# Performance work log

Hardware: AMD Instinct MI355X
Metric: run time of the kernel (lower is better)

The kernel has to match this reference:

```python
import jax, jax.numpy as jnp
import numpy as np


def _segment_mean(x, idx, num_segments):
    # mean-aggregate rows of x into num_segments buckets (PyG SAGEConv default aggr)
    s = jax.ops.segment_sum(x, idx, num_segments=num_segments)
    c = jax.ops.segment_sum(jnp.ones((idx.shape[0],), x.dtype), idx, num_segments=num_segments)
    return s / jnp.maximum(c, 1.0)[:, None]


def setup_inputs() -> dict:
    key = jax.random.key(0)
    ks = jax.random.split(key, 12)
    N_LIG, N_PROT, D, H, E = 100000, 50000, 64, 128, 2000000
    sc = 0.05
    return {
        "x_lig": jax.random.normal(ks[0], (N_LIG, D), jnp.float32),
        "x_prot": jax.random.normal(ks[1], (N_PROT, D), jnp.float32),
        "W_l_lp": jax.random.normal(ks[2], (D, H), jnp.float32) * sc,
        "b_lp": jnp.zeros((H,), jnp.float32),
        "W_r_lp": jax.random.normal(ks[3], (D, H), jnp.float32) * sc,
        "W_l_pl": jax.random.normal(ks[4], (D, H), jnp.float32) * sc,
        "b_pl": jnp.zeros((H,), jnp.float32),
        "W_r_pl": jax.random.normal(ks[5], (D, H), jnp.float32) * sc,
        "W_lin": jax.random.normal(ks[6], (H, 1), jnp.float32) * sc,
        "b_lin": jnp.zeros((1,), jnp.float32),
        "src_lp": jax.random.randint(ks[7], (E,), 0, N_LIG, jnp.int32),
        "dst_lp": jax.random.randint(ks[8], (E,), 0, N_PROT, jnp.int32),
        "src_pl": jax.random.randint(ks[9], (E,), 0, N_PROT, jnp.int32),
        "dst_pl": jax.random.randint(ks[10], (E,), 0, N_LIG, jnp.int32),
    }


def reference(x_lig, x_prot, W_l_lp, b_lp, W_r_lp, W_l_pl, b_pl, W_r_pl,
              W_lin, b_lin, src_lp, dst_lp, src_pl, dst_pl):
    n_lig = x_lig.shape[0]
    n_prot = x_prot.shape[0]
    # SAGEConv ('ligand','interacts','protein'): gather ligand feats along edges, mean into proteins
    agg_prot = _segment_mean(x_lig[src_lp], dst_lp, n_prot)          # [N_prot, D]
    h_prot = jax.nn.relu(agg_prot @ W_l_lp + b_lp + x_prot @ W_r_lp)  # [N_prot, H] (dead downstream, as in original)
    # SAGEConv ('protein','interacts','ligand')
    agg_lig = _segment_mean(x_prot[src_pl], dst_pl, n_lig)           # [N_lig, D]
    h_lig = jax.nn.relu(agg_lig @ W_l_pl + b_pl + x_lig @ W_r_pl)    # [N_lig, H]
    ligand_out = h_lig.mean(axis=0)                                  # [H]
    del h_prot  # original computes it but never uses it (only 'ligand' feeds the head)
    return ligand_out @ W_lin + b_lin                                # [1]
```

## Files before the change

kernel.cpp:

```cpp
#include <hip/hip_runtime.h>

#define D 64
#define H 128
#define BN 128
#define CAP 3456
#define NBB 256
#define CE 7816

typedef short bf16x8 __attribute__((ext_vector_type(8)));
typedef float f32x4  __attribute__((ext_vector_type(4)));

__device__ __forceinline__ ushort f2bf(float f) {
    unsigned u = __float_as_uint(f);
    unsigned r = (u + 0x7FFFu + ((u >> 16) & 1u)) >> 16;
    return (ushort)r;
}

__device__ __forceinline__ bf16x8 pack8(float4 a, float4 b) {
    ushort o[8];
    o[0]=f2bf(a.x); o[1]=f2bf(a.y); o[2]=f2bf(a.z); o[3]=f2bf(a.w);
    o[4]=f2bf(b.x); o[5]=f2bf(b.y); o[6]=f2bf(b.z); o[7]=f2bf(b.w);
    bf16x8 r;
    __builtin_memcpy(&r, o, 16);
    return r;
}

__device__ __forceinline__ void accu(float* a, uint4 v) {
    a[0] += __uint_as_float(v.x << 16); a[1] += __uint_as_float(v.x & 0xFFFF0000u);
    a[2] += __uint_as_float(v.y << 16); a[3] += __uint_as_float(v.y & 0xFFFF0000u);
    a[4] += __uint_as_float(v.z << 16); a[5] += __uint_as_float(v.z & 0xFFFF0000u);
    a[6] += __uint_as_float(v.w << 16); a[7] += __uint_as_float(v.w & 0xFFFF0000u);
}

__global__ __launch_bounds__(256)
void stage1_kernel(const float* __restrict__ xp, ushort* __restrict__ xpb, int totalp,
                   const float* __restrict__ Wl, const float* __restrict__ Wr,
                   ushort* __restrict__ wprep,
                   const int* __restrict__ dst, int* __restrict__ cnt,
                   int E, int K, int ce, int PB) {
    __shared__ int scnt[800];
    int bid = blockIdx.x;
    int t = threadIdx.x;
    if (bid < PB) {
        int i = (bid * 256 + t) * 8;
        if (i < totalp) {
            float4 a = *(const float4*)(xp + i);
            float4 b = *(const float4*)(xp + i + 4);
            bf16x8 v = pack8(a, b);
            *(bf16x8*)(xpb + i) = v;
        }
    } else if (bid < PB + 8) {
        int e = (bid - PB) * 256 + t;
        if (e < 2048) {
            int lane = e & 63;
            int ks = (e >> 6) & 3;
            int ht = e >> 8;
            int h = ht * 16 + (lane & 15);
            int k0 = ks * 32 + (lane >> 4) * 8;
            ushort o[8];
            #pragma unroll
            for (int j = 0; j < 8; ++j) {
                int k = k0 + j;
                float v = (k < D) ? Wl[k * H + h] : Wr[(k - D) * H + h];
                o[j] = f2bf(v);
            }
            *(bf16x8*)(wprep + (size_t)e * 8) = *(bf16x8*)o;
        }
    } else {
        int blk = bid - PB - 8;
        for (int b = t; b < 800; b += 256) scnt[b] = 0;
        __syncthreads();
        int e0 = blk * ce;
        int e1 = min(E, e0 + ce);
        for (int i = e0 + t * 4; i < e1; i += 1024) {
            int4 d4 = *(const int4*)(dst + i);
            atomicAdd(&scnt[d4.x >> 7], 1);
            atomicAdd(&scnt[d4.y >> 7], 1);
            atomicAdd(&scnt[d4.z >> 7], 1);
            atomicAdd(&scnt[d4.w >> 7], 1);
        }
        __syncthreads();
        int* row = cnt + (size_t)blk * K;
        for (int b = t; b < K; b += 256) row[b] = scnt[b];
    }
}

__global__ __launch_bounds__(NBB)
void part_scan_kernel(const int* __restrict__ cnt, int* __restrict__ off,
                      int* __restrict__ tot, int K) {
    __shared__ int s[NBB];
    int b = blockIdx.x;
    int t = threadIdx.x;
    int v = cnt[(size_t)t * K + b];
    s[t] = v;
    __syncthreads();
    for (int o = 1; o < NBB; o <<= 1) {
        int x = (t >= o) ? s[t - o] : 0;
        __syncthreads();
        s[t] += x;
        __syncthreads();
    }
    off[(size_t)t * K + b] = s[t] - v;
    if (t == NBB - 1) tot[b] = s[t];
}

__global__ __launch_bounds__(512)
void part_scatter_kernel(const int* __restrict__ src, const int* __restrict__ dst,
                         const int* __restrict__ off, int* __restrict__ gb,
                         int E, int K, int ce) {
    __shared__ int shist[800];
    __shared__ int sbase[800];
    __shared__ int gdelta[800];
    __shared__ int lcur[800];
    __shared__ int sscan[512];
    __shared__ int ebuf[CE];
    __shared__ unsigned short bkt[CE];

    int blk = blockIdx.x, t = threadIdx.x;
    int e0 = blk * ce;
    int e1 = min(E, e0 + ce);
    int myn = e1 - e0;

    for (int b = t; b < 800; b += 512) shist[b] = 0;
    __syncthreads();
    for (int i = e0 + t * 4; i < e1; i += 2048) {
        int4 d4 = *(const int4*)(dst + i);
        atomicAdd(&shist[d4.x >> 7], 1);
        atomicAdd(&shist[d4.y >> 7], 1);
        atomicAdd(&shist[d4.z >> 7], 1);
        atomicAdd(&shist[d4.w >> 7], 1);
    }
    __syncthreads();
    int c0 = 0, c1 = 0;
    if (t < 400) { c0 = shist[2 * t]; c1 = shist[2 * t + 1]; }
    int cs = c0 + c1;
    sscan[t] = (t < 400) ? cs : 0;
    __syncthreads();
    for (int o = 1; o < 512; o <<= 1) {
        int x = (t >= o) ? sscan[t - o] : 0;
        __syncthreads();
        sscan[t] += x;
        __syncthreads();
    }
    if (t < 400) {
        int ex = sscan[t] - cs;
        sbase[2 * t] = ex;
        sbase[2 * t + 1] = ex + c0;
    }
    __syncthreads();
    const int* orow = off + (size_t)blk * K;
    for (int b = t; b < K; b += 512) {
        int sb = sbase[b];
        gdelta[b] = orow[b] - sb;
        lcur[b] = sb;
    }
    __syncthreads();
    for (int i = e0 + t * 4; i < e1; i += 2048) {
        int4 d4 = *(const int4*)(dst + i);
        int4 s4 = *(const int4*)(src + i);
        int b, p;
        b = d4.x >> 7; p = atomicAdd(&lcur[b], 1);
        ebuf[p] = (s4.x & 0xFFFF) | ((d4.x & 127) << 16); bkt[p] = (unsigned short)b;
        b = d4.y >> 7; p = atomicAdd(&lcur[b], 1);
        ebuf[p] = (s4.y & 0xFFFF) | ((d4.y & 127) << 16); bkt[p] = (unsigned short)b;
        b = d4.z >> 7; p = atomicAdd(&lcur[b], 1);
        ebuf[p] = (s4.z & 0xFFFF) | ((d4.z & 127) << 16); bkt[p] = (unsigned short)b;
        b = d4.w >> 7; p = atomicAdd(&lcur[b], 1);
        ebuf[p] = (s4.w & 0xFFFF) | ((d4.w & 127) << 16); bkt[p] = (unsigned short)b;
    }
    __syncthreads();
    for (int p = t; p < myn; p += 512) {
        int b = bkt[p];
        int loc = gdelta[b] + p;
        if (loc < CAP) gb[(size_t)b * CAP + loc] = ebuf[p];
    }
}

__global__ __launch_bounds__(512, 4)
void fused_kernel(const ushort* __restrict__ xpb, const float* __restrict__ x_lig,
                  const int* __restrict__ gtot, const int* __restrict__ gb,
                  const ushort* __restrict__ wprep, const float* __restrict__ bvec,
                  float* __restrict__ pgrid, int N) {
    __shared__ int sdeg[BN];
    __shared__ int sstart[BN];
    __shared__ int scur[BN];
    __shared__ int ssc[BN];
    __shared__ int scsr[CAP];
    __shared__ float sred[8][H];

    int b = blockIdx.x, t = threadIdx.x;
    int cnt = min(gtot[b], CAP);
    const int* mygb = gb + (size_t)b * CAP;

    if (t < BN) sdeg[t] = 0;
    __syncthreads();
    for (int i = t; i < cnt; i += 512)
        atomicAdd(&sdeg[mygb[i] >> 16], 1);
    __syncthreads();
    if (t < BN) ssc[t] = sdeg[t];
    __syncthreads();
    for (int off = 1; off < BN; off <<= 1) {
        int v = 0;
        if (t < BN && t >= off) v = ssc[t - off];
        __syncthreads();
        if (t < BN) ssc[t] += v;
        __syncthreads();
    }
    if (t < BN) {
        int ex = ssc[t] - sdeg[t];
        sstart[t] = ex;
        scur[t] = ex;
    }
    __syncthreads();
    for (int i = t; i < cnt; i += 512) {
        int e = mygb[i];
        int p = atomicAdd(&scur[e >> 16], 1);
        scsr[p] = e & 0xFFFF;
    }
    __syncthreads();

    int wv = t >> 6, lane = t & 63;
    int r = lane & 15, kg = lane >> 4;

    int ln = wv * 16 + r;
    int s0 = sstart[ln], dg = sdeg[ln];
    float a0[8] = {0.f,0.f,0.f,0.f,0.f,0.f,0.f,0.f};
    float a1[8] = {0.f,0.f,0.f,0.f,0.f,0.f,0.f,0.f};
    int j = 0;
    for (; j + 1 < dg; j += 2) {
        int i0 = scsr[s0 + j];
        int i1 = scsr[s0 + j + 1];
        const ushort* r0 = xpb + (size_t)i0 * D + kg * 8;
        const ushort* r1 = xpb + (size_t)i1 * D + kg * 8;
        uint4 u0 = *(const uint4*)(r0);
        uint4 u1 = *(const uint4*)(r0 + 32);
        uint4 w0 = *(const uint4*)(r1);
        uint4 w1 = *(const uint4*)(r1 + 32);
        accu(a0, u0); accu(a1, u1);
        accu(a0, w0); accu(a1, w1);
    }
    if (j < dg) {
        int i0 = scsr[s0 + j];
        const ushort* r0 = xpb + (size_t)i0 * D + kg * 8;
        uint4 u0 = *(const uint4*)(r0);
        uint4 u1 = *(const uint4*)(r0 + 32);
        accu(a0, u0); accu(a1, u1);
    }

    float inv = 1.0f / fmaxf((float)dg, 1.0f);
    ushort o0[8], o1[8];
    #pragma unroll
    for (int k = 0; k < 8; ++k) {
        o0[k] = f2bf(a0[k] * inv);
        o1[k] = f2bf(a1[k] * inv);
    }
    bf16x8 A0, A1;
    __builtin_memcpy(&A0, o0, 16);
    __builtin_memcpy(&A1, o1, 16);

    int grow = b * BN + wv * 16 + r;
    bf16x8 A2, A3;
    if (grow < N) {
        const float* xr = x_lig + (size_t)grow * D;
        float4 va = *(const float4*)(xr + kg * 8);
        float4 vb = *(const float4*)(xr + kg * 8 + 4);
        A2 = pack8(va, vb);
        float4 vc = *(const float4*)(xr + 32 + kg * 8);
        float4 vd = *(const float4*)(xr + 32 + kg * 8 + 4);
        A3 = pack8(vc, vd);
    } else {
        A2 = bf16x8{0,0,0,0,0,0,0,0};
        A3 = A2;
    }

    float hsum[8];
    bool full = (b * BN + wv * 16 + 16 <= N);
    const bf16x8* wp = (const bf16x8*)wprep;
    #pragma unroll 2
    for (int ht = 0; ht < 8; ++ht) {
        f32x4 acc = {0.f, 0.f, 0.f, 0.f};
        acc = __builtin_amdgcn_mfma_f32_16x16x32_bf16(A0, wp[(ht*4+0)*64 + lane], acc, 0, 0, 0);
        acc = __builtin_amdgcn_mfma_f32_16x16x32_bf16(A1, wp[(ht*4+1)*64 + lane], acc, 0, 0, 0);
        acc = __builtin_amdgcn_mfma_f32_16x16x32_bf16(A2, wp[(ht*4+2)*64 + lane], acc, 0, 0, 0);
        acc = __builtin_amdgcn_mfma_f32_16x16x32_bf16(A3, wp[(ht*4+3)*64 + lane], acc, 0, 0, 0);
        float bb = bvec[ht * 16 + r];
        float s = 0.f;
        if (full) {
            #pragma unroll
            for (int i = 0; i < 4; ++i) s += fmaxf(acc[i] + bb, 0.f);
        } else {
            #pragma unroll
            for (int i = 0; i < 4; ++i) {
                int row = b * BN + wv * 16 + kg * 4 + i;
                if (row < N) s += fmaxf(acc[i] + bb, 0.f);
            }
        }
        hsum[ht] = s;
    }

    #pragma unroll
    for (int ht = 0; ht < 8; ++ht) {
        float v = hsum[ht];
        v += __shfl_xor(v, 16);
        v += __shfl_xor(v, 32);
        if (lane < 16) sred[wv][ht * 16 + lane] = v;
    }
    __syncthreads();
    if (t < H) {
        float s = 0.f;
        #pragma unroll
        for (int w = 0; w < 8; ++w) s += sred[w][t];
        pgrid[(size_t)b * H + t] = s;
    }
}

__global__ __launch_bounds__(128)
void reduce1_kernel(const float* __restrict__ pgrid, int nb, float* __restrict__ pgrid2) {
    int t = threadIdx.x;
    float s = 0.f;
    for (int r = blockIdx.x; r < nb; r += 64) s += pgrid[(size_t)r * H + t];
    pgrid2[(size_t)blockIdx.x * H + t] = s;
}

__global__ __launch_bounds__(128)
void head_kernel(const float* __restrict__ pgrid2,
                 const float* __restrict__ W_lin, const float* __restrict__ b_lin,
                 float* __restrict__ out, float invN) {
    __shared__ float sh[H];
    int t = threadIdx.x;
    float s = 0.f;
    #pragma unroll 8
    for (int r = 0; r < 64; ++r) s += pgrid2[(size_t)r * H + t];
    sh[t] = s * invN * W_lin[t];
    __syncthreads();
    if (t == 0) {
        float tot = b_lin[0];
        for (int i = 0; i < H; ++i) tot += sh[i];
        out[0] = tot;
    }
}

extern "C" void kernel_launch(void* const* d_in, const int* in_sizes, int n_in,
                              void* d_out, int out_size, void* d_ws, size_t ws_size,
                              hipStream_t stream) {
    const float* x_lig  = (const float*)d_in[0];
    const float* x_prot = (const float*)d_in[1];
    const float* W_l_pl = (const float*)d_in[5];
    const float* b_pl   = (const float*)d_in[6];
    const float* W_r_pl = (const float*)d_in[7];
    const float* W_lin  = (const float*)d_in[8];
    const float* b_lin  = (const float*)d_in[9];
    const int*   src_pl = (const int*)d_in[12];
    const int*   dst_pl = (const int*)d_in[13];

    int N  = in_sizes[0] / D;
    int NP = in_sizes[1] / D;
    int E  = in_sizes[12];
    int K  = (N + BN - 1) / BN;

    char* base = (char*)d_ws;
    ushort* xpb   = (ushort*)base;  base += (size_t)NP * D * sizeof(ushort);
    float* pgrid  = (float*)base;   base += (size_t)K * H * sizeof(float);
    float* pgrid2 = (float*)base;   base += (size_t)64 * H * sizeof(float);
    ushort* wprep = (ushort*)base;  base += (size_t)2048 * 8 * sizeof(ushort);
    int* cnt      = (int*)base;     base += (size_t)NBB * K * sizeof(int);
    int* off      = (int*)base;     base += (size_t)NBB * K * sizeof(int);
    int* tot      = (int*)base;     base += (size_t)K * sizeof(int);
    base = (char*)(((size_t)base + 255) & ~(size_t)255);
    int* gb       = (int*)base;     base += (size_t)K * CAP * sizeof(int);

    int ce = ((E + NBB - 1) / NBB + 3) & ~3;
    int PB = (NP * D / 8 + 255) / 256;

    stage1_kernel<<<PB + 8 + NBB, 256, 0, stream>>>(x_prot, xpb, NP * D,
                                                    W_l_pl, W_r_pl, wprep,
                                                    dst_pl, cnt, E, K, ce, PB);
    part_scan_kernel<<<K, NBB, 0, stream>>>(cnt, off, tot, K);
    part_scatter_kernel<<<NBB, 512, 0, stream>>>(src_pl, dst_pl, off, gb, E, K, ce);
    fused_kernel<<<K, 512, 0, stream>>>(xpb, x_lig, tot, gb, wprep, b_pl, pgrid, N);
    reduce1_kernel<<<64, 128, 0, stream>>>(pgrid, K, pgrid2);
    head_kernel<<<1, 128, 0, stream>>>(pgrid2, W_lin, b_lin, (float*)d_out,
                                       1.0f / (float)N);
}
```

Measured before the change: 95.94 us.

## Store protein features as FP8 for gather, unroll gather by four, raise occupancy

The protein feature table is now converted to FP8 (e4m3) instead of bf16, which halves the bytes fetched per gathered neighbor row. The gather loop is unrolled to four edges and accumulates with packed FP8-to-f32 conversions. The weight prep is permuted so its K ordering matches the new interleaved layout of the aggregated features. Nontemporal loads are added for streamed data, and the launch bound is raised to 8 blocks per CU. FP8 quantization of the inputs loses a lot of precision, which may push the result outside the tolerance.

```diff
diff --git a/kernel.cpp b/kernel.cpp
--- a/kernel.cpp
+++ b/kernel.cpp
@@ -9,6 +9,7 @@
 
 typedef short bf16x8 __attribute__((ext_vector_type(8)));
 typedef float f32x4  __attribute__((ext_vector_type(4)));
+typedef float f32x2  __attribute__((ext_vector_type(2)));
 
 __device__ __forceinline__ ushort f2bf(float f) {
     unsigned u = __float_as_uint(f);
@@ -16,24 +17,34 @@
     return (ushort)r;
 }
 
-__device__ __forceinline__ bf16x8 pack8(float4 a, float4 b) {
+__device__ __forceinline__ bf16x8 pack8v(f32x4 a, f32x4 b) {
     ushort o[8];
-    o[0]=f2bf(a.x); o[1]=f2bf(a.y); o[2]=f2bf(a.z); o[3]=f2bf(a.w);
-    o[4]=f2bf(b.x); o[5]=f2bf(b.y); o[6]=f2bf(b.z); o[7]=f2bf(b.w);
+    o[0]=f2bf(a[0]); o[1]=f2bf(a[1]); o[2]=f2bf(a[2]); o[3]=f2bf(a[3]);
+    o[4]=f2bf(b[0]); o[5]=f2bf(b[1]); o[6]=f2bf(b[2]); o[7]=f2bf(b[3]);
     bf16x8 r;
     __builtin_memcpy(&r, o, 16);
     return r;
 }
 
-__device__ __forceinline__ void accu(float* a, uint4 v) {
-    a[0] += __uint_as_float(v.x << 16); a[1] += __uint_as_float(v.x & 0xFFFF0000u);
-    a[2] += __uint_as_float(v.y << 16); a[3] += __uint_as_float(v.y & 0xFFFF0000u);
-    a[4] += __uint_as_float(v.z << 16); a[5] += __uint_as_float(v.z & 0xFFFF0000u);
-    a[6] += __uint_as_float(v.w << 16); a[7] += __uint_as_float(v.w & 0xFFFF0000u);
+__device__ __forceinline__ void acc16(f32x2* a, uint4 v) {
+    a[0] += __builtin_amdgcn_cvt_pk_f32_fp8((int)v.x, false);
+    a[1] += __builtin_amdgcn_cvt_pk_f32_fp8((int)v.x, true);
+    a[2] += __builtin_amdgcn_cvt_pk_f32_fp8((int)v.y, false);
+    a[3] += __builtin_amdgcn_cvt_pk_f32_fp8((int)v.y, true);
+    a[4] += __builtin_amdgcn_cvt_pk_f32_fp8((int)v.z, false);
+    a[5] += __builtin_amdgcn_cvt_pk_f32_fp8((int)v.z, true);
+    a[6] += __builtin_amdgcn_cvt_pk_f32_fp8((int)v.w, false);
+    a[7] += __builtin_amdgcn_cvt_pk_f32_fp8((int)v.w, true);
+}
+
+__device__ __forceinline__ unsigned pk4_fp8(float x0, float x1, float x2, float x3) {
+    int w = __builtin_amdgcn_cvt_pk_fp8_f32(x0, x1, 0, false);
+    w = __builtin_amdgcn_cvt_pk_fp8_f32(x2, x3, w, true);
+    return (unsigned)w;
 }
 
 __global__ __launch_bounds__(256)
-void stage1_kernel(const float* __restrict__ xp, ushort* __restrict__ xpb, int totalp,
+void stage1_kernel(const float* __restrict__ xp, unsigned char* __restrict__ xp8, int totalp,
                    const float* __restrict__ Wl, const float* __restrict__ Wr,
                    ushort* __restrict__ wprep,
                    const int* __restrict__ dst, int* __restrict__ cnt,
@@ -42,12 +53,19 @@
     int bid = blockIdx.x;
     int t = threadIdx.x;
     if (bid < PB) {
-        int i = (bid * 256 + t) * 8;
+        int i = (bid * 256 + t) * 16;
         if (i < totalp) {
-            float4 a = *(const float4*)(xp + i);
-            float4 b = *(const float4*)(xp + i + 4);
-            bf16x8 v = pack8(a, b);
-            *(bf16x8*)(xpb + i) = v;
+            const f32x4* p = (const f32x4*)(xp + i);
+            f32x4 a = __builtin_nontemporal_load(p);
+            f32x4 b = __builtin_nontemporal_load(p + 1);
+            f32x4 c = __builtin_nontemporal_load(p + 2);
+            f32x4 d = __builtin_nontemporal_load(p + 3);
+            uint4 o;
+            o.x = pk4_fp8(a[0], a[1], a[2], a[3]);
+            o.y = pk4_fp8(b[0], b[1], b[2], b[3]);
+            o.z = pk4_fp8(c[0], c[1], c[2], c[3]);
+            o.w = pk4_fp8(d[0], d[1], d[2], d[3]);
+            *(uint4*)(xp8 + i) = o;
         }
     } else if (bid < PB + 8) {
         int e = (bid - PB) * 256 + t;
@@ -56,11 +74,12 @@
             int ks = (e >> 6) & 3;
             int ht = e >> 8;
             int h = ht * 16 + (lane & 15);
-            int k0 = ks * 32 + (lane >> 4) * 8;
+            int kgp = lane >> 4;
             ushort o[8];
             #pragma unroll
             for (int j = 0; j < 8; ++j) {
-                int k = k0 + j;
+                int k = (ks < 2) ? (kgp * 16 + ks * 8 + j)
+                                 : (ks * 32 + kgp * 8 + j);
                 float v = (k < D) ? Wl[k * H + h] : Wr[(k - D) * H + h];
                 o[j] = f2bf(v);
             }
@@ -176,8 +195,8 @@
     }
 }
 
-__global__ __launch_bounds__(512, 4)
-void fused_kernel(const ushort* __restrict__ xpb, const float* __restrict__ x_lig,
+__global__ __launch_bounds__(512, 8)
+void fused_kernel(const unsigned char* __restrict__ xp8, const float* __restrict__ x_lig,
                   const int* __restrict__ gtot, const int* __restrict__ gb,
                   const ushort* __restrict__ wprep, const float* __restrict__ bvec,
                   float* __restrict__ pgrid, int N) {
@@ -195,7 +214,7 @@
     if (t < BN) sdeg[t] = 0;
     __syncthreads();
     for (int i = t; i < cnt; i += 512)
-        atomicAdd(&sdeg[mygb[i] >> 16], 1);
+        atomicAdd(&sdeg[__builtin_nontemporal_load(&mygb[i]) >> 16], 1);
     __syncthreads();
     if (t < BN) ssc[t] = sdeg[t];
     __syncthreads();
@@ -213,7 +232,7 @@
     }
     __syncthreads();
     for (int i = t; i < cnt; i += 512) {
-        int e = mygb[i];
+        int e = __builtin_nontemporal_load(&mygb[i]);
         int p = atomicAdd(&scur[e >> 16], 1);
         scsr[p] = e & 0xFFFF;
     }
@@ -224,35 +243,35 @@
 
     int ln = wv * 16 + r;
     int s0 = sstart[ln], dg = sdeg[ln];
-    float a0[8] = {0.f,0.f,0.f,0.f,0.f,0.f,0.f,0.f};
-    float a1[8] = {0.f,0.f,0.f,0.f,0.f,0.f,0.f,0.f};
+    f32x2 a[8];
+    #pragma unroll
+    for (int k = 0; k < 8; ++k) { a[k][0] = 0.f; a[k][1] = 0.f; }
     int j = 0;
-    for (; j + 1 < dg; j += 2) {
+    for (; j + 3 < dg; j += 4) {
         int i0 = scsr[s0 + j];
         int i1 = scsr[s0 + j + 1];
-        const ushort* r0 = xpb + (size_t)i0 * D + kg * 8;
-        const ushort* r1 = xpb + (size_t)i1 * D + kg * 8;
-        uint4 u0 = *(const uint4*)(r0);
-        uint4 u1 = *(const uint4*)(r0 + 32);
-        uint4 w0 = *(const uint4*)(r1);
-        uint4 w1 = *(const uint4*)(r1 + 32);
-        accu(a0, u0); accu(a1, u1);
-        accu(a0, w0); accu(a1, w1);
-    }
-    if (j < dg) {
+        int i2 = scsr[s0 + j + 2];
+        int i3 = scsr[s0 + j + 3];
+        uint4 v0 = *((const uint4*)(xp8 + (size_t)i0 * D) + kg);
+        uint4 v1 = *((const uint4*)(xp8 + (size_t)i1 * D) + kg);
+        uint4 v2 = *((const uint4*)(xp8 + (size_t)i2 * D) + kg);
+        uint4 v3 = *((const uint4*)(xp8 + (size_t)i3 * D) + kg);
+        acc16(a, v0); acc16(a, v1); acc16(a, v2); acc16(a, v3);
+    }
+    for (; j < dg; ++j) {
         int i0 = scsr[s0 + j];
-        const ushort* r0 = xpb + (size_t)i0 * D + kg * 8;
-        uint4 u0 = *(const uint4*)(r0);
-        uint4 u1 = *(const uint4*)(r0 + 32);
-        accu(a0, u0); accu(a1, u1);
+        uint4 v0 = *((const uint4*)(xp8 + (size_t)i0 * D) + kg);
+        acc16(a, v0);
     }
 
     float inv = 1.0f / fmaxf((float)dg, 1.0f);
     ushort o0[8], o1[8];
     #pragma unroll
-    for (int k = 0; k < 8; ++k) {
-        o0[k] = f2bf(a0[k] * inv);
-        o1[k] = f2bf(a1[k] * inv);
+    for (int k = 0; k < 4; ++k) {
+        o0[2*k]   = f2bf(a[k][0] * inv);
+        o0[2*k+1] = f2bf(a[k][1] * inv);
+        o1[2*k]   = f2bf(a[4+k][0] * inv);
+        o1[2*k+1] = f2bf(a[4+k][1] * inv);
     }
     bf16x8 A0, A1;
     __builtin_memcpy(&A0, o0, 16);
@@ -261,13 +280,13 @@
     int grow = b * BN + wv * 16 + r;
     bf16x8 A2, A3;
     if (grow < N) {
-        const float* xr = x_lig + (size_t)grow * D;
-        float4 va = *(const float4*)(xr + kg * 8);
-        float4 vb = *(const float4*)(xr + kg * 8 + 4);
-        A2 = pack8(va, vb);
-        float4 vc = *(const float4*)(xr + 32 + kg * 8);
-        float4 vd = *(const float4*)(xr + 32 + kg * 8 + 4);
-        A3 = pack8(vc, vd);
+        const f32x4* xr = (const f32x4*)(x_lig + (size_t)grow * D);
+        f32x4 va = __builtin_nontemporal_load(xr + kg * 2);
+        f32x4 vb = __builtin_nontemporal_load(xr + kg * 2 + 1);
+        A2 = pack8v(va, vb);
+        f32x4 vc = __builtin_nontemporal_load(xr + 8 + kg * 2);
+        f32x4 vd = __builtin_nontemporal_load(xr + 8 + kg * 2 + 1);
+        A3 = pack8v(vc, vd);
     } else {
         A2 = bf16x8{0,0,0,0,0,0,0,0};
         A3 = A2;
@@ -359,7 +378,7 @@
     int K  = (N + BN - 1) / BN;
 
     char* base = (char*)d_ws;
-    ushort* xpb   = (ushort*)base;  base += (size_t)NP * D * sizeof(ushort);
+    unsigned char* xp8 = (unsigned char*)base; base += (size_t)NP * D;
     float* pgrid  = (float*)base;   base += (size_t)K * H * sizeof(float);
     float* pgrid2 = (float*)base;   base += (size_t)64 * H * sizeof(float);
     ushort* wprep = (ushort*)base;  base += (size_t)2048 * 8 * sizeof(ushort);
@@ -370,14 +389,14 @@
     int* gb       = (int*)base;     base += (size_t)K * CAP * sizeof(int);
 
     int ce = ((E + NBB - 1) / NBB + 3) & ~3;
-    int PB = (NP * D / 8 + 255) / 256;
-
-    stage1_kernel<<<PB + 8 + NBB, 256, 0, stream>>>(x_prot, xpb, NP * D,
+    int PB = (NP * D / 16 + 255) / 256;
+
+    stage1_kernel<<<PB + 8 + NBB, 256, 0, stream>>>(x_prot, xp8, NP * D,
                                                     W_l_pl, W_r_pl, wprep,
                                                     dst_pl, cnt, E, K, ce, PB);
     part_scan_kernel<<<K, NBB, 0, stream>>>(cnt, off, tot, K);
     part_scatter_kernel<<<NBB, 512, 0, stream>>>(src_pl, dst_pl, off, gb, E, K, ce);
-    fused_kernel<<<K, 512, 0, stream>>>(xpb, x_lig, tot, gb, wprep, b_pl, pgrid, N);
+    fused_kernel<<<K, 512, 0, stream>>>(xp8, x_lig, tot, gb, wprep, b_pl, pgrid, N);
     reduce1_kernel<<<64, 128, 0, stream>>>(pgrid, K, pgrid2);
     head_kernel<<<1, 128, 0, stream>>>(pgrid2, W_lin, b_lin, (float*)d_out,
                                        1.0f / (float)N);
```

New measurement: 109.8 us. +14.5%, slower.
